# Optimization experiments

Hardware: AMD Instinct MI355X
Metric: run time of the kernel (lower is better)

Reference implementation:

```python
import jax, jax.numpy as jnp
import numpy as np
import math

H = 16  # num heads
NEG = -1e9


def setup_inputs() -> dict:
    key = jax.random.key(0)
    ks = jax.random.split(key, 12)
    B, S, D = 2, 2048, 1024
    inp = {
        "query": jax.random.normal(ks[0], (B, S, D), jnp.float32),
        "key": jax.random.normal(ks[1], (B, S, D), jnp.float32),
        "value": jax.random.normal(ks[2], (B, S, D), jnp.float32),
        "mask": jax.random.randint(ks[3], (B, 1, S), 0, 2, jnp.int32),
        "wq": jax.random.normal(ks[4], (D, D), jnp.float32) * 0.02,
        "bq": jnp.zeros((D,), jnp.float32),
        "wk": jax.random.normal(ks[5], (D, D), jnp.float32) * 0.02,
        "bk": jnp.zeros((D,), jnp.float32),
        "wv": jax.random.normal(ks[6], (D, D), jnp.float32) * 0.02,
        "bv": jnp.zeros((D,), jnp.float32),
        "wo": jax.random.normal(ks[7], (D, D), jnp.float32) * 0.02,
        "bo": jnp.zeros((D,), jnp.float32),
    }
    return inp


def reference(query, key, value, mask, wq, bq, wk, bk, wv, bv, wo, bo):
    B, S, D = query.shape
    dk = D // H

    def proj(x, w, b):
        # torch Linear: x @ w.T + b ; then split heads -> [B, H, S, dk]
        y = x @ w.T + b
        return y.reshape(B, -1, H, dk).transpose(0, 2, 1, 3)

    q = proj(query, wq, bq)
    k = proj(key, wk, bk)
    v = proj(value, wv, bv)

    scores = jnp.einsum("bhqd,bhkd->bhqk", q, k) / math.sqrt(dk)  # [B,H,S,S]

    m = mask[:, None, :, :]  # [B,1,1,S] (mask.unsqueeze(1) in torch)
    scores = jnp.where(m == 0, NEG, scores)            # key-side padding mask
    scores = jnp.where(jnp.swapaxes(m, -2, -1) == 0, NEG, scores)  # query-side mask (q_len>1)

    p_attn = jax.nn.softmax(scores, axis=-1)
    # dropout p=0 / eval mode -> identity
    ctx = jnp.einsum("bhqk,bhkd->bhqd", p_attn, v)  # [B,H,S,dk]
    ctx = ctx.transpose(0, 2, 1, 3).reshape(B, S, H * dk)
    out = ctx @ wo.T + bo
    return out
```

## Files before the change

### kernel.cpp

```cpp
#include <hip/hip_runtime.h>
#include <hip/hip_bf16.h>

#define SEQ 2048
#define DIM 1024
#define NH  16
#define DK  64
#define NA  (2 * SEQ * DIM)
#define NW  (DIM * DIM)
#define PSTR 72
#define TSTR 132
#define QSCALE 0.18033688011112042f

typedef __attribute__((ext_vector_type(4))) float f32x4;
typedef __attribute__((ext_vector_type(8))) __bf16 bf16x8;
typedef __attribute__((ext_vector_type(4))) __bf16 bf16x4;

__device__ __forceinline__ f32x4 mfma16(bf16x8 a, bf16x8 b, f32x4 c) {
  return __builtin_amdgcn_mfma_f32_16x16x32_bf16(a, b, c, 0, 0, 0);
}
__device__ __forceinline__ void async_load16(const void* g, void* l) {
  __builtin_amdgcn_global_load_lds(
      (const __attribute__((address_space(1))) void*)g,
      (__attribute__((address_space(3))) void*)l, 16, 0, 0);
}
__device__ __forceinline__ int swz(int row, int chunk) {
  return row * 8 + (chunk ^ (row & 7));
}

__global__ __launch_bounds__(256) void cvt_kernel(
    const float* __restrict__ s0, const float* __restrict__ s1,
    const float* __restrict__ s2, const float* __restrict__ s3,
    const float* __restrict__ s4, const float* __restrict__ s5,
    const float* __restrict__ s6,
    __hip_bfloat16* __restrict__ d0, __hip_bfloat16* __restrict__ d1,
    __hip_bfloat16* __restrict__ d2, __hip_bfloat16* __restrict__ d3,
    __hip_bfloat16* __restrict__ d4, __hip_bfloat16* __restrict__ d5,
    __hip_bfloat16* __restrict__ d6) {
  const int t = blockIdx.y;
  const float* s;
  __hip_bfloat16* d;
  int n;
  switch (t) {
    case 0: s = s0; d = d0; n = NA; break;
    case 1: s = s1; d = d1; n = NA; break;
    case 2: s = s2; d = d2; n = NA; break;
    case 3: s = s3; d = d3; n = NW; break;
    case 4: s = s4; d = d4; n = NW; break;
    case 5: s = s5; d = d5; n = NW; break;
    default: s = s6; d = d6; n = NW; break;
  }
  size_t i = ((size_t)blockIdx.x * 256 + threadIdx.x) * 8;
  if (i >= (size_t)n) return;
  float4 a = *(const float4*)(s + i);
  float4 b = *(const float4*)(s + i + 4);
  bf16x8 v = {(__bf16)a.x, (__bf16)a.y, (__bf16)a.z, (__bf16)a.w,
              (__bf16)b.x, (__bf16)b.y, (__bf16)b.z, (__bf16)b.w};
  *(bf16x8*)(d + i) = v;
}

__device__ __forceinline__ void gemm_mainloop(
    const __hip_bfloat16* __restrict__ X, const __hip_bfloat16* __restrict__ W,
    __hip_bfloat16* A_lds, __hip_bfloat16* B_lds, int m0, int n0,
    f32x4 acc[4][4]) {
  const int K = DIM;
  const int tid = threadIdx.x, lane = tid & 63, w = tid >> 6;
  const int quad = lane >> 4, l15 = lane & 15;
  const int wm = (w >> 1) * 64, wn = (w & 1) * 64;

  f32x4 z = {0.f, 0.f, 0.f, 0.f};
  for (int mi = 0; mi < 4; ++mi)
    for (int ni = 0; ni < 4; ++ni) acc[mi][ni] = z;

  for (int k0 = 0; k0 < K; k0 += 64) {
    for (int r = 0; r < 4; ++r) {
      int cbase = r * 256 + w * 64;
      int c = cbase + lane, row = c >> 3, cs = c & 7;
      int off = cs ^ (row & 7);
      async_load16((const char*)(X + (size_t)(m0 + row) * K + k0) + off * 16,
                   (char*)A_lds + cbase * 16);
      async_load16((const char*)(W + (size_t)(n0 + row) * K + k0) + off * 16,
                   (char*)B_lds + cbase * 16);
    }
    __syncthreads();
    for (int kk = 0; kk < 2; ++kk) {
      bf16x8 a[4], b[4];
      for (int mi = 0; mi < 4; ++mi)
        a[mi] = *(const bf16x8*)(A_lds + swz(wm + mi * 16 + l15, kk * 4 + quad) * 8);
      for (int ni = 0; ni < 4; ++ni)
        b[ni] = *(const bf16x8*)(B_lds + swz(wn + ni * 16 + l15, kk * 4 + quad) * 8);
      for (int mi = 0; mi < 4; ++mi)
        for (int ni = 0; ni < 4; ++ni)
          acc[mi][ni] = mfma16(a[mi], b[ni], acc[mi][ni]);
    }
    __syncthreads();
  }
}

__global__ __launch_bounds__(256) void qkv_proj_kernel(
    const __hip_bfloat16* __restrict__ xq, const __hip_bfloat16* __restrict__ xk,
    const __hip_bfloat16* __restrict__ xv,
    const __hip_bfloat16* __restrict__ wq, const __hip_bfloat16* __restrict__ wk,
    const __hip_bfloat16* __restrict__ wv,
    const float* __restrict__ bq, const float* __restrict__ bk,
    const float* __restrict__ bv,
    __hip_bfloat16* __restrict__ q_ws, __hip_bfloat16* __restrict__ k_ws,
    __hip_bfloat16* __restrict__ vt_ws) {
  __shared__ __align__(16) __hip_bfloat16 S_lds[128 * TSTR];

  const int z = blockIdx.z;
  const __hip_bfloat16* X = (z == 0) ? xq : ((z == 1) ? xk : xv);
  const __hip_bfloat16* W = (z == 0) ? wq : ((z == 1) ? wk : wv);
  const float* bias = (z == 0) ? bq : ((z == 1) ? bk : bv);
  const float f = (z == 0) ? QSCALE : 1.0f;

  const int m0 = blockIdx.y * 128, n0 = blockIdx.x * 128;
  f32x4 acc[4][4];
  gemm_mainloop(X, W, S_lds, S_lds + 128 * 64, m0, n0, acc);

  const int tid = threadIdx.x, lane = tid & 63, w = tid >> 6;
  const int quad = lane >> 4, l15 = lane & 15;
  const int wm = (w >> 1) * 64, wn = (w & 1) * 64;

  if (z != 2) {
    __hip_bfloat16* out = (z == 0) ? q_ws : k_ws;
    for (int mi = 0; mi < 4; ++mi)
      for (int ni = 0; ni < 4; ++ni) {
        const int n = n0 + wn + ni * 16 + l15;
        const float bv_ = bias[n];
        const int h = n >> 6, d = n & 63;
        for (int r = 0; r < 4; ++r) {
          const int m = m0 + wm + mi * 16 + quad * 4 + r;
          const int b = m >> 11, s = m & 2047;
          out[((size_t)(b * NH + h) * SEQ + s) * DK + d] =
              __float2bfloat16((acc[mi][ni][r] + bv_) * f);
        }
      }
  } else {
    for (int mi = 0; mi < 4; ++mi)
      for (int ni = 0; ni < 4; ++ni) {
        const int n_local = wn + ni * 16 + l15;
        const float bv_ = bias[n0 + n_local];
        bf16x4 tv;
        for (int r = 0; r < 4; ++r) tv[r] = (__bf16)(acc[mi][ni][r] + bv_);
        *(bf16x4*)(S_lds + n_local * TSTR + wm + mi * 16 + quad * 4) = tv;
      }
    __syncthreads();
    const int b = m0 >> 11, s_base = m0 & 2047;
    for (int r2 = 0; r2 < 8; ++r2) {
      int c2 = r2 * 256 + tid;
      int nrow = c2 >> 4, moff = (c2 & 15) * 8;
      int n = n0 + nrow, h = n >> 6, d = n & 63;
      *(uint4*)(vt_ws + ((size_t)(b * NH + h) * DK + d) * SEQ + s_base + moff) =
          *(const uint4*)(S_lds + nrow * TSTR + moff);
    }
  }
}

__global__ __launch_bounds__(512) void attn_kernel(
    const __hip_bfloat16* __restrict__ qg, const __hip_bfloat16* __restrict__ kg,
    const __hip_bfloat16* __restrict__ vtg, const int* __restrict__ mask,
    __hip_bfloat16* __restrict__ ctx) {
  __shared__ __align__(16) __hip_bfloat16 QP_lds[128 * PSTR];
  __shared__ __align__(16) __hip_bfloat16 K_lds[64 * 64];
  __shared__ __align__(16) __hip_bfloat16 V_lds[64 * 64];
  __shared__ float bias_lds[SEQ];

  const int tid = threadIdx.x, lane = tid & 63, w = tid >> 6;
  const int quad = lane >> 4, l15 = lane & 15;
  const int bh = blockIdx.y, b = bh >> 4, h = bh & 15;
  const int q0 = blockIdx.x * 128;
  const size_t head = (size_t)bh * SEQ * DK;

  for (int i = tid; i < SEQ; i += 512)
    bias_lds[i] = mask[b * SEQ + i] ? 0.f : -1e9f;

  for (int r = 0; r < 2; ++r) {
    int cbase = r * 512 + w * 64;
    int c = cbase + lane, row = c >> 3, cs = c & 7;
    int off = cs ^ (row & 7);
    async_load16((const char*)(qg + head + (size_t)(q0 + row) * DK) + off * 16,
                 (char*)QP_lds + cbase * 16);
  }
  __syncthreads();

  bf16x8 qf[2];
  for (int kk = 0; kk < 2; ++kk)
    qf[kk] = *(const bf16x8*)(QP_lds + swz(w * 16 + l15, kk * 4 + quad) * 8);
  const int qmv = mask[b * SEQ + q0 + w * 16 + l15];

  __hip_bfloat16* P_lds = QP_lds;
  const bf16x8 ones = {(__bf16)1.f, (__bf16)1.f, (__bf16)1.f, (__bf16)1.f,
                       (__bf16)1.f, (__bf16)1.f, (__bf16)1.f, (__bf16)1.f};

  f32x4 z = {0.f, 0.f, 0.f, 0.f};
  f32x4 o_acc[4];
  for (int di = 0; di < 4; ++di) o_acc[di] = z;
  f32x4 o_sum = z;

  for (int t = 0; t < 32; ++t) {
    const int k0 = t * 64;
    {
      int c = tid, row = c >> 3, cs = c & 7;
      int off = cs ^ (row & 7);
      async_load16((const char*)(kg + head + (size_t)(k0 + row) * DK) + off * 16,
                   (char*)K_lds + c * 16);
      async_load16(
          (const char*)(vtg + (size_t)bh * DK * SEQ + (size_t)row * SEQ + k0) + off * 16,
          (char*)V_lds + c * 16);
    }
    __syncthreads();

    f32x4 s_acc[4];
    for (int mi = 0; mi < 4; ++mi)
      s_acc[mi] = *(const f32x4*)(bias_lds + k0 + mi * 16 + quad * 4);
    for (int kk = 0; kk < 2; ++kk) {
      bf16x8 ak[4];
      for (int mi = 0; mi < 4; ++mi)
        ak[mi] = *(const bf16x8*)(K_lds + swz(mi * 16 + l15, kk * 4 + quad) * 8);
      for (int mi = 0; mi < 4; ++mi)
        s_acc[mi] = mfma16(ak[mi], qf[kk], s_acc[mi]);
    }

    for (int mi = 0; mi < 4; ++mi) {
      bf16x4 pk;
      for (int r = 0; r < 4; ++r) {
        float s2 = qmv ? s_acc[mi][r] : 0.f;
        pk[r] = (__bf16)__builtin_amdgcn_exp2f(s2);
      }
      *(bf16x4*)(P_lds + (w * 16 + l15) * PSTR + mi * 16 + quad * 4) = pk;
    }

    for (int kk = 0; kk < 2; ++kk) {
      bf16x8 bp = *(const bf16x8*)(P_lds + (w * 16 + l15) * PSTR + kk * 32 + quad * 8);
      bf16x8 av[4];
      for (int di = 0; di < 4; ++di)
        av[di] = *(const bf16x8*)(V_lds + swz(di * 16 + l15, kk * 4 + quad) * 8);
      for (int di = 0; di < 4; ++di)
        o_acc[di] = mfma16(av[di], bp, o_acc[di]);
      o_sum = mfma16(ones, bp, o_sum);
    }
    __syncthreads();
  }

  const float inv = 1.f / o_sum[0];

  for (int di = 0; di < 4; ++di) {
    bf16x4 ov;
    for (int r = 0; r < 4; ++r) ov[r] = (__bf16)(o_acc[di][r] * inv);
    *(bf16x4*)(P_lds + (w * 16 + l15) * PSTR + di * 16 + quad * 4) = ov;
  }
  __syncthreads();
  for (int r = 0; r < 2; ++r) {
    int c = r * 512 + tid, row = c >> 3, off = c & 7;
    *(uint4*)(ctx + (size_t)(b * SEQ + q0 + row) * DIM + h * DK + off * 8) =
        *(const uint4*)(P_lds + row * PSTR + off * 8);
  }
}

__global__ __launch_bounds__(256) void out_proj_kernel(
    const __hip_bfloat16* __restrict__ ctx, const __hip_bfloat16* __restrict__ wo,
    const float* __restrict__ bo, float* __restrict__ out) {
  __shared__ __align__(16) __hip_bfloat16 A_lds[128 * 64];
  __shared__ __align__(16) __hip_bfloat16 B_lds[128 * 64];

  const int m0 = blockIdx.y * 128, n0 = blockIdx.x * 128;
  f32x4 acc[4][4];
  gemm_mainloop(ctx, wo, A_lds, B_lds, m0, n0, acc);

  const int tid = threadIdx.x, lane = tid & 63, w = tid >> 6;
  const int quad = lane >> 4, l15 = lane & 15;
  const int wm = (w >> 1) * 64, wn = (w & 1) * 64;

  for (int mi = 0; mi < 4; ++mi)
    for (int ni = 0; ni < 4; ++ni) {
      const int n = n0 + wn + ni * 16 + l15;
      const float bv_ = bo[n];
      for (int r = 0; r < 4; ++r) {
        const int m = m0 + wm + mi * 16 + quad * 4 + r;
        out[(size_t)m * DIM + n] = acc[mi][ni][r] + bv_;
      }
    }
}

extern "C" void kernel_launch(void* const* d_in, const int* in_sizes, int n_in,
                              void* d_out, int out_size, void* d_ws, size_t ws_size,
                              hipStream_t stream) {
  const float* query = (const float*)d_in[0];
  const float* key   = (const float*)d_in[1];
  const float* value = (const float*)d_in[2];
  const int*   mask  = (const int*)d_in[3];
  const float* wq = (const float*)d_in[4];
  const float* bq = (const float*)d_in[5];
  const float* wk = (const float*)d_in[6];
  const float* bk = (const float*)d_in[7];
  const float* wv = (const float*)d_in[8];
  const float* bv = (const float*)d_in[9];
  const float* wo = (const float*)d_in[10];
  const float* bo = (const float*)d_in[11];
  float* out = (float*)d_out;

  char* ws = (char*)d_ws;
  const size_t SZA = (size_t)NA * 2;
  const size_t SZW = (size_t)NW * 2;
  __hip_bfloat16* xq  = (__hip_bfloat16*)(ws);
  __hip_bfloat16* xk  = (__hip_bfloat16*)(ws + SZA);
  __hip_bfloat16* xv  = (__hip_bfloat16*)(ws + 2 * SZA);
  __hip_bfloat16* wqb = (__hip_bfloat16*)(ws + 3 * SZA);
  __hip_bfloat16* wkb = (__hip_bfloat16*)(ws + 3 * SZA + SZW);
  __hip_bfloat16* wvb = (__hip_bfloat16*)(ws + 3 * SZA + 2 * SZW);
  __hip_bfloat16* wob = (__hip_bfloat16*)(ws + 3 * SZA + 3 * SZW);
  __hip_bfloat16* q_ws  = (__hip_bfloat16*)(ws + 3 * SZA + 4 * SZW);
  __hip_bfloat16* k_ws  = (__hip_bfloat16*)(ws + 4 * SZA + 4 * SZW);
  __hip_bfloat16* vt_ws = (__hip_bfloat16*)(ws + 5 * SZA + 4 * SZW);
  __hip_bfloat16* ctx_ws = xq;

  cvt_kernel<<<dim3(2048, 7), dim3(256), 0, stream>>>(
      query, key, value, wq, wk, wv, wo, xq, xk, xv, wqb, wkb, wvb, wob);
  qkv_proj_kernel<<<dim3(8, 32, 3), dim3(256), 0, stream>>>(
      xq, xk, xv, wqb, wkb, wvb, bq, bk, bv, q_ws, k_ws, vt_ws);
  attn_kernel<<<dim3(16, 32), dim3(512), 0, stream>>>(q_ws, k_ws, vt_ws, mask, ctx_ws);
  out_proj_kernel<<<dim3(8, 32), dim3(256), 0, stream>>>(ctx_ws, wob, bo, out);
}
```

Baseline: 239.6 us.

## Stage GEMM epilogues through LDS, double-buffer attention K/V, compact cvt grid

```diff
diff --git a/kernel.cpp b/kernel.cpp
--- a/kernel.cpp
+++ b/kernel.cpp
@@ -8,7 +8,8 @@
 #define NA  (2 * SEQ * DIM)
 #define NW  (DIM * DIM)
 #define PSTR 72
-#define TSTR 132
+#define ESTR 136
+#define FSTR 132
 #define QSCALE 0.18033688011112042f
 
 typedef __attribute__((ext_vector_type(4))) float f32x4;
@@ -36,21 +37,22 @@
     __hip_bfloat16* __restrict__ d2, __hip_bfloat16* __restrict__ d3,
     __hip_bfloat16* __restrict__ d4, __hip_bfloat16* __restrict__ d5,
     __hip_bfloat16* __restrict__ d6) {
-  const int t = blockIdx.y;
+  const int id = blockIdx.x;
   const float* s;
   __hip_bfloat16* d;
-  int n;
-  switch (t) {
-    case 0: s = s0; d = d0; n = NA; break;
-    case 1: s = s1; d = d1; n = NA; break;
-    case 2: s = s2; d = d2; n = NA; break;
-    case 3: s = s3; d = d3; n = NW; break;
-    case 4: s = s4; d = d4; n = NW; break;
-    case 5: s = s5; d = d5; n = NW; break;
-    default: s = s6; d = d6; n = NW; break;
-  }
-  size_t i = ((size_t)blockIdx.x * 256 + threadIdx.x) * 8;
-  if (i >= (size_t)n) return;
+  int bid;
+  if (id < 6144) {
+    int t = id >> 11;
+    bid = id & 2047;
+    s = (t == 0) ? s0 : ((t == 1) ? s1 : s2);
+    d = (t == 0) ? d0 : ((t == 1) ? d1 : d2);
+  } else {
+    int t = (id - 6144) >> 9;
+    bid = (id - 6144) & 511;
+    s = (t == 0) ? s3 : ((t == 1) ? s4 : ((t == 2) ? s5 : s6));
+    d = (t == 0) ? d3 : ((t == 1) ? d4 : ((t == 2) ? d5 : d6));
+  }
+  size_t i = ((size_t)bid * 256 + threadIdx.x) * 8;
   float4 a = *(const float4*)(s + i);
   float4 b = *(const float4*)(s + i + 4);
   bf16x8 v = {(__bf16)a.x, (__bf16)a.y, (__bf16)a.z, (__bf16)a.w,
@@ -105,7 +107,7 @@
     const float* __restrict__ bv,
     __hip_bfloat16* __restrict__ q_ws, __hip_bfloat16* __restrict__ k_ws,
     __hip_bfloat16* __restrict__ vt_ws) {
-  __shared__ __align__(16) __hip_bfloat16 S_lds[128 * TSTR];
+  __shared__ __align__(16) __hip_bfloat16 S_lds[128 * ESTR];
 
   const int z = blockIdx.z;
   const __hip_bfloat16* X = (z == 0) ? xq : ((z == 1) ? xk : xv);
@@ -123,18 +125,27 @@
 
   if (z != 2) {
     __hip_bfloat16* out = (z == 0) ? q_ws : k_ws;
-    for (int mi = 0; mi < 4; ++mi)
-      for (int ni = 0; ni < 4; ++ni) {
-        const int n = n0 + wn + ni * 16 + l15;
-        const float bv_ = bias[n];
-        const int h = n >> 6, d = n & 63;
-        for (int r = 0; r < 4; ++r) {
-          const int m = m0 + wm + mi * 16 + quad * 4 + r;
-          const int b = m >> 11, s = m & 2047;
-          out[((size_t)(b * NH + h) * SEQ + s) * DK + d] =
-              __float2bfloat16((acc[mi][ni][r] + bv_) * f);
-        }
+    for (int p = 0; p < 2; ++p) {
+      if ((w >> 1) == p) {
+        for (int mi = 0; mi < 4; ++mi)
+          for (int ni = 0; ni < 4; ++ni) {
+            const float bv_ = bias[n0 + wn + ni * 16 + l15];
+            for (int r = 0; r < 4; ++r)
+              S_lds[(mi * 16 + quad * 4 + r) * ESTR + wn + ni * 16 + l15] =
+                  __float2bfloat16((acc[mi][ni][r] + bv_) * f);
+          }
       }
+      __syncthreads();
+      for (int r2 = 0; r2 < 4; ++r2) {
+        int c = r2 * 256 + tid;
+        int row = c >> 4, j = c & 15;
+        int m = m0 + p * 64 + row, b = m >> 11, s = m & 2047;
+        int n = n0 + j * 8, h = n >> 6, d = n & 63;
+        *(uint4*)(out + ((size_t)(b * NH + h) * SEQ + s) * DK + d) =
+            *(const uint4*)(S_lds + row * ESTR + j * 8);
+      }
+      __syncthreads();
+    }
   } else {
     for (int mi = 0; mi < 4; ++mi)
       for (int ni = 0; ni < 4; ++ni) {
@@ -142,7 +153,7 @@
         const float bv_ = bias[n0 + n_local];
         bf16x4 tv;
         for (int r = 0; r < 4; ++r) tv[r] = (__bf16)(acc[mi][ni][r] + bv_);
-        *(bf16x4*)(S_lds + n_local * TSTR + wm + mi * 16 + quad * 4) = tv;
+        *(bf16x4*)(S_lds + n_local * ESTR + wm + mi * 16 + quad * 4) = tv;
       }
     __syncthreads();
     const int b = m0 >> 11, s_base = m0 & 2047;
@@ -151,7 +162,7 @@
       int nrow = c2 >> 4, moff = (c2 & 15) * 8;
       int n = n0 + nrow, h = n >> 6, d = n & 63;
       *(uint4*)(vt_ws + ((size_t)(b * NH + h) * DK + d) * SEQ + s_base + moff) =
-          *(const uint4*)(S_lds + nrow * TSTR + moff);
+          *(const uint4*)(S_lds + nrow * ESTR + moff);
     }
   }
 }
@@ -161,8 +172,8 @@
     const __hip_bfloat16* __restrict__ vtg, const int* __restrict__ mask,
     __hip_bfloat16* __restrict__ ctx) {
   __shared__ __align__(16) __hip_bfloat16 QP_lds[128 * PSTR];
-  __shared__ __align__(16) __hip_bfloat16 K_lds[64 * 64];
-  __shared__ __align__(16) __hip_bfloat16 V_lds[64 * 64];
+  __shared__ __align__(16) __hip_bfloat16 K_lds[2][64 * 64];
+  __shared__ __align__(16) __hip_bfloat16 V_lds[2][64 * 64];
   __shared__ float bias_lds[SEQ];
 
   const int tid = threadIdx.x, lane = tid & 63, w = tid >> 6;
@@ -170,6 +181,7 @@
   const int bh = blockIdx.y, b = bh >> 4, h = bh & 15;
   const int q0 = blockIdx.x * 128;
   const size_t head = (size_t)bh * SEQ * DK;
+  const size_t vthead = (size_t)bh * DK * SEQ;
 
   for (int i = tid; i < SEQ; i += 512)
     bias_lds[i] = mask[b * SEQ + i] ? 0.f : -1e9f;
@@ -181,6 +193,14 @@
     async_load16((const char*)(qg + head + (size_t)(q0 + row) * DK) + off * 16,
                  (char*)QP_lds + cbase * 16);
   }
+  {
+    int row = tid >> 3, cs = tid & 7;
+    int off = cs ^ (row & 7);
+    async_load16((const char*)(kg + head + (size_t)row * DK) + off * 16,
+                 (char*)K_lds[0] + tid * 16);
+    async_load16((const char*)(vtg + vthead + (size_t)row * SEQ) + off * 16,
+                 (char*)V_lds[0] + tid * 16);
+  }
   __syncthreads();
 
   bf16x8 qf[2];
@@ -198,17 +218,17 @@
   f32x4 o_sum = z;
 
   for (int t = 0; t < 32; ++t) {
+    const int cur = t & 1;
+    if (t < 31) {
+      const int k1 = (t + 1) * 64;
+      int row = tid >> 3, cs = tid & 7;
+      int off = cs ^ (row & 7);
+      async_load16((const char*)(kg + head + (size_t)(k1 + row) * DK) + off * 16,
+                   (char*)K_lds[1 - cur] + tid * 16);
+      async_load16((const char*)(vtg + vthead + (size_t)row * SEQ + k1) + off * 16,
+                   (char*)V_lds[1 - cur] + tid * 16);
+    }
     const int k0 = t * 64;
-    {
-      int c = tid, row = c >> 3, cs = c & 7;
-      int off = cs ^ (row & 7);
-      async_load16((const char*)(kg + head + (size_t)(k0 + row) * DK) + off * 16,
-                   (char*)K_lds + c * 16);
-      async_load16(
-          (const char*)(vtg + (size_t)bh * DK * SEQ + (size_t)row * SEQ + k0) + off * 16,
-          (char*)V_lds + c * 16);
-    }
-    __syncthreads();
 
     f32x4 s_acc[4];
     for (int mi = 0; mi < 4; ++mi)
@@ -216,7 +236,7 @@
     for (int kk = 0; kk < 2; ++kk) {
       bf16x8 ak[4];
       for (int mi = 0; mi < 4; ++mi)
-        ak[mi] = *(const bf16x8*)(K_lds + swz(mi * 16 + l15, kk * 4 + quad) * 8);
+        ak[mi] = *(const bf16x8*)(K_lds[cur] + swz(mi * 16 + l15, kk * 4 + quad) * 8);
       for (int mi = 0; mi < 4; ++mi)
         s_acc[mi] = mfma16(ak[mi], qf[kk], s_acc[mi]);
     }
@@ -234,7 +254,7 @@
       bf16x8 bp = *(const bf16x8*)(P_lds + (w * 16 + l15) * PSTR + kk * 32 + quad * 8);
       bf16x8 av[4];
       for (int di = 0; di < 4; ++di)
-        av[di] = *(const bf16x8*)(V_lds + swz(di * 16 + l15, kk * 4 + quad) * 8);
+        av[di] = *(const bf16x8*)(V_lds[cur] + swz(di * 16 + l15, kk * 4 + quad) * 8);
       for (int di = 0; di < 4; ++di)
         o_acc[di] = mfma16(av[di], bp, o_acc[di]);
       o_sum = mfma16(ones, bp, o_sum);
@@ -260,26 +280,36 @@
 __global__ __launch_bounds__(256) void out_proj_kernel(
     const __hip_bfloat16* __restrict__ ctx, const __hip_bfloat16* __restrict__ wo,
     const float* __restrict__ bo, float* __restrict__ out) {
-  __shared__ __align__(16) __hip_bfloat16 A_lds[128 * 64];
-  __shared__ __align__(16) __hip_bfloat16 B_lds[128 * 64];
+  __shared__ __align__(16) __hip_bfloat16 S_lds[64 * FSTR * 2];
 
   const int m0 = blockIdx.y * 128, n0 = blockIdx.x * 128;
   f32x4 acc[4][4];
-  gemm_mainloop(ctx, wo, A_lds, B_lds, m0, n0, acc);
+  gemm_mainloop(ctx, wo, S_lds, S_lds + 128 * 64, m0, n0, acc);
 
   const int tid = threadIdx.x, lane = tid & 63, w = tid >> 6;
   const int quad = lane >> 4, l15 = lane & 15;
-  const int wm = (w >> 1) * 64, wn = (w & 1) * 64;
-
-  for (int mi = 0; mi < 4; ++mi)
-    for (int ni = 0; ni < 4; ++ni) {
-      const int n = n0 + wn + ni * 16 + l15;
-      const float bv_ = bo[n];
-      for (int r = 0; r < 4; ++r) {
-        const int m = m0 + wm + mi * 16 + quad * 4 + r;
-        out[(size_t)m * DIM + n] = acc[mi][ni][r] + bv_;
-      }
-    }
+  const int wn = (w & 1) * 64;
+  float* epi = (float*)S_lds;
+
+  for (int p = 0; p < 2; ++p) {
+    if ((w >> 1) == p) {
+      for (int mi = 0; mi < 4; ++mi)
+        for (int ni = 0; ni < 4; ++ni) {
+          const float bv_ = bo[n0 + wn + ni * 16 + l15];
+          for (int r = 0; r < 4; ++r)
+            epi[(mi * 16 + quad * 4 + r) * FSTR + wn + ni * 16 + l15] =
+                acc[mi][ni][r] + bv_;
+        }
+    }
+    __syncthreads();
+    for (int r2 = 0; r2 < 8; ++r2) {
+      int c = r2 * 256 + tid;
+      int row = c >> 5, j = c & 31;
+      *(float4*)(out + (size_t)(m0 + p * 64 + row) * DIM + n0 + j * 4) =
+          *(const float4*)(epi + row * FSTR + j * 4);
+    }
+    __syncthreads();
+  }
 }
 
 extern "C" void kernel_launch(void* const* d_in, const int* in_sizes, int n_in,
@@ -314,7 +344,7 @@
   __hip_bfloat16* vt_ws = (__hip_bfloat16*)(ws + 5 * SZA + 4 * SZW);
   __hip_bfloat16* ctx_ws = xq;
 
-  cvt_kernel<<<dim3(2048, 7), dim3(256), 0, stream>>>(
+  cvt_kernel<<<dim3(8192), dim3(256), 0, stream>>>(
       query, key, value, wq, wk, wv, wo, xq, xk, xv, wqb, wkb, wvb, wob);
   qkv_proj_kernel<<<dim3(8, 32, 3), dim3(256), 0, stream>>>(
       xq, xk, xv, wqb, wkb, wvb, bq, bk, bv, q_ws, k_ws, vt_ws);
```

After: 238.5 us. No clear change (-0.4%).
